# Optimization experiments

Hardware: AMD Instinct MI355X
Metric: run time of the kernel (lower is better)

The kernel has to match this reference:

```python
import jax, jax.numpy as jnp
import numpy as np

NUM_EMBEDDINGS = 1024
EMBEDDING_DIM = 256
COMMITMENT_COST = 0.25


def setup_inputs() -> dict:
    key = jax.random.key(0)
    k1, k2 = jax.random.split(key)
    inputs = jax.random.normal(k1, (64, 1024, EMBEDDING_DIM), dtype=jnp.float32)
    # codebook initialized uniform(-1/K, 1/K) as in the torch module
    embedding = jax.random.uniform(
        k2, (NUM_EMBEDDINGS, EMBEDDING_DIM), dtype=jnp.float32,
        minval=-1.0 / NUM_EMBEDDINGS, maxval=1.0 / NUM_EMBEDDINGS)
    return {"inputs": inputs, "embedding": embedding}


def reference(inputs, embedding):
    # flatten to [N, D]
    D = embedding.shape[1]
    flat = inputs.reshape(-1, D)
    distances = (jnp.sum(flat * flat, axis=1, keepdims=True)
                 + jnp.sum(embedding * embedding, axis=1)
                 - 2.0 * jnp.matmul(flat, embedding.T))
    encoding_indices = jnp.argmin(distances, axis=1)  # [N]
    # one_hot @ embedding == gather; use gather (same math, no NxK one-hot)
    quantized = jnp.take(embedding, encoding_indices, axis=0).reshape(inputs.shape)
    # commitment loss: mse(stop_grad(quantized), inputs)
    e_latent_loss = jnp.mean(jnp.square(jax.lax.stop_gradient(quantized) - inputs))
    loss = COMMITMENT_COST * e_latent_loss
    # straight-through estimator
    quantized = inputs + jax.lax.stop_gradient(quantized - inputs)
    return quantized, loss, encoding_indices.reshape(inputs.shape[:-1])
```

## Files before the change

kernel.cpp:

```cpp
#include <hip/hip_runtime.h>
#include <cfloat>
#include <climits>

#define N_ROWS 65536
#define DIM 256
#define K_CODES 1024
#define N_ELEM 16777216
#define OUT_LOSS_OFF 16777216
#define OUT_IDX_OFF  16777217

#define ROWS_PB 128
#define CT 128
#define EPS_MARGIN 1.5e-4f
#define SHORTLIST_EPS 6e-4f
#define RB 8

#define WS_PARTIALS 0
#define WS_ESQ      8192
#define WS_IDX      12288
#define WS_FLAGCNT  274432
#define WS_FLAGLIST 274436
#define WS_EHI      540672
#define WS_ELO      1064960
#define WS_EHIT     1589248

typedef unsigned short u16;
typedef __attribute__((ext_vector_type(8))) short bf16x8;
typedef __attribute__((ext_vector_type(4))) float f32x4;
typedef union { bf16x8 v; unsigned u[4]; } frag_u;

__device__ __forceinline__ void glds16(const void* g, void* l) {
    __builtin_amdgcn_global_load_lds(
        (const __attribute__((address_space(1))) unsigned int*)g,
        (__attribute__((address_space(3))) unsigned int*)l,
        16, 0, 0);
}

__device__ __forceinline__ unsigned cvt_pk_bf16(float lo, float hi) {
    unsigned r;
    asm("v_cvt_pk_bf16_f32 %0, %1, %2" : "=v"(r) : "v"(lo), "v"(hi));
    return r;
}

__device__ __forceinline__ void split8(float4 a, float4 b, bf16x8& h8, bf16x8& l8) {
    frag_u H, L;
    float f0 = a.x, f1 = a.y, f2 = a.z, f3 = a.w;
    float f4 = b.x, f5 = b.y, f6 = b.z, f7 = b.w;
    const float* f[8] = {&f0,&f1,&f2,&f3,&f4,&f5,&f6,&f7};
    #pragma unroll
    for (int p = 0; p < 4; ++p) {
        float xl = *f[2*p], xh = *f[2*p+1];
        unsigned hw = cvt_pk_bf16(xl, xh);
        float hfl = __uint_as_float(hw << 16);
        float hfh = __uint_as_float(hw & 0xffff0000u);
        H.u[p] = hw;
        L.u[p] = cvt_pk_bf16(xl - hfl, xh - hfh);
    }
    h8 = H.v; l8 = L.v;
}

__device__ __forceinline__ void bsplit(float x, u16& h, u16& l) {
    unsigned u = __float_as_uint(x);
    unsigned hb = (u + 0x7fffu + ((u >> 16) & 1u)) >> 16;
    h = (u16)hb;
    float hf = __uint_as_float(hb << 16);
    float lf = x - hf;
    unsigned u2 = __float_as_uint(lf);
    l = (u16)((u2 + 0x7fffu + ((u2 >> 16) & 1u)) >> 16);
}

__device__ __forceinline__ float np_pairwise_sumsq(const float* __restrict__ a) {
    float half[2];
    #pragma unroll
    for (int h = 0; h < 2; ++h) {
        const float* p = a + h * 128;
        float r[8];
        #pragma unroll
        for (int j = 0; j < 8; ++j) r[j] = __fmul_rn(p[j], p[j]);
        for (int i = 8; i < 128; i += 8) {
            #pragma unroll
            for (int j = 0; j < 8; ++j)
                r[j] = __fadd_rn(r[j], __fmul_rn(p[i + j], p[i + j]));
        }
        half[h] = __fadd_rn(__fadd_rn(__fadd_rn(r[0], r[1]), __fadd_rn(r[2], r[3])),
                            __fadd_rn(__fadd_rn(r[4], r[5]), __fadd_rn(r[6], r[7])));
    }
    return __fadd_rn(half[0], half[1]);
}

__launch_bounds__(256)
__global__ void eprep_kernel(const float* __restrict__ e, u16* __restrict__ ehi,
                             u16* __restrict__ elo, u16* __restrict__ ehiT,
                             float* __restrict__ esqOut, int* __restrict__ flagCnt) {
    const int b = blockIdx.x;
    if (b < 256) {
        int i4 = b * 256 + threadIdx.x;
        float4 v = ((const float4*)e)[i4];
        ushort4 h, l;
        bsplit(v.x, h.x, l.x); bsplit(v.y, h.y, l.y);
        bsplit(v.z, h.z, l.z); bsplit(v.w, h.w, l.w);
        ((ushort4*)ehi)[i4] = h;
        ((ushort4*)elo)[i4] = l;
        int c = i4 >> 6;
        int f4 = i4 & 63;
        int qid = f4 >> 1;
        ((ushort4*)ehiT)[((size_t)qid * 1024 + c) * 2 + (f4 & 1)] = h;
    } else {
        if (b == 256 && threadIdx.x == 0) *flagCnt = 0;
        int c = (b - 256) * 256 + threadIdx.x;
        if (c < K_CODES) esqOut[c] = np_pairwise_sumsq(e + c * DIM);
    }
}

__launch_bounds__(512, 4)
__global__ void argmin_kernel(const float* __restrict__ x,
                              const u16* __restrict__ ehi, const u16* __restrict__ elo,
                              const float* __restrict__ esq, int* __restrict__ wsIdx,
                              int* __restrict__ flagCnt, int* __restrict__ flagList) {
    __shared__ __align__(16) unsigned char lds[65536];
    __shared__ float esq_s[CT];
    u16* xhiS = (u16*)lds;
    u16* xloS = (u16*)(lds + 16384);
    u16* ehiS = (u16*)(lds + 32768);
    u16* eloS = (u16*)(lds + 49152);

    const int t = threadIdx.x;
    const int w = t >> 6;
    const int l = t & 63;
    const int lane15 = l & 15;
    const int quad = l >> 4;
    const int rowBase = blockIdx.x * ROWS_PB;
    const int wr = w >> 1;
    const int wc = w & 1;

    float bv[8], sv[8]; int bi[8];
    #pragma unroll
    for (int i = 0; i < 8; ++i) { bv[i] = FLT_MAX; sv[i] = FLT_MAX; bi[i] = INT_MAX; }

    const int sub8 = l >> 3;
    const int jb8 = l & 7;
    const int sb8 = jb8 ^ sub8;
    const u16* srcE = (w < 6) ? ehi : elo;
    u16* dstE = (w < 6) ? ehiS : eloS;
    const int halfE = w & 1;

    const int g0 = t;
    const int g1 = 512 + t;
    const int r0 = g0 >> 3, jb0 = g0 & 7, sb0 = jb0 ^ (r0 & 7);
    const int r1 = g1 >> 3, jb1 = g1 & 7, sb1 = jb1 ^ (r1 & 7);

    for (int ct = 0; ct < 8; ++ct) {
        const int ctBase = ct * CT;
        __syncthreads();
        if (t < CT) esq_s[t] = esq[ctBase + t];

        f32x4 acc[2][4];
        #pragma unroll
        for (int ti = 0; ti < 2; ++ti)
            #pragma unroll
            for (int tj = 0; tj < 4; ++tj) acc[ti][tj] = (f32x4){0.f, 0.f, 0.f, 0.f};

        for (int ch = 0; ch < 4; ++ch) {
            __syncthreads();
            const float4* gp0 = (const float4*)(x + (size_t)(rowBase + r0) * 256 + ch * 64 + sb0 * 8);
            const float4* gp1 = (const float4*)(x + (size_t)(rowBase + r1) * 256 + ch * 64 + sb1 * 8);
            float4 va0 = gp0[0], vb0 = gp0[1];
            float4 va1 = gp1[0], vb1 = gp1[1];
            if (w >= 4) {
                #pragma unroll
                for (int i = 0; i < 8; ++i) {
                    int r = halfE * 64 + i * 8 + sub8;
                    glds16(srcE + (size_t)(ctBase + r) * 256 + ch * 64 + sb8 * 8,
                           dstE + halfE * 4096 + i * 512);
                }
            }
            {
                bf16x8 h8, l8;
                split8(va0, vb0, h8, l8);
                *(bf16x8*)(xhiS + r0 * 64 + jb0 * 8) = h8;
                *(bf16x8*)(xloS + r0 * 64 + jb0 * 8) = l8;
                split8(va1, vb1, h8, l8);
                *(bf16x8*)(xhiS + r1 * 64 + jb1 * 8) = h8;
                *(bf16x8*)(xloS + r1 * 64 + jb1 * 8) = l8;
            }
            __syncthreads();

            #pragma unroll
            for (int kk = 0; kk < 2; ++kk) {
                bf16x8 ah[2], al4[2], bh[4], bl[4];
                const int blk = kk * 4 + quad;
                #pragma unroll
                for (int ti = 0; ti < 2; ++ti) {
                    int r = wr * 32 + ti * 16 + lane15;
                    int off = r * 64 + ((blk ^ (r & 7)) * 8);
                    ah[ti]  = *(const bf16x8*)(xhiS + off);
                    al4[ti] = *(const bf16x8*)(xloS + off);
                }
                #pragma unroll
                for (int tj = 0; tj < 4; ++tj) {
                    int r = wc * 64 + tj * 16 + lane15;
                    int off = r * 64 + ((blk ^ (r & 7)) * 8);
                    bh[tj] = *(const bf16x8*)(ehiS + off);
                    bl[tj] = *(const bf16x8*)(eloS + off);
                }
                #pragma unroll
                for (int ti = 0; ti < 2; ++ti)
                    #pragma unroll
                    for (int tj = 0; tj < 4; ++tj) {
                        acc[ti][tj] = __builtin_amdgcn_mfma_f32_16x16x32_bf16(al4[ti], bh[tj], acc[ti][tj], 0, 0, 0);
                        acc[ti][tj] = __builtin_amdgcn_mfma_f32_16x16x32_bf16(ah[ti], bl[tj], acc[ti][tj], 0, 0, 0);
                        acc[ti][tj] = __builtin_amdgcn_mfma_f32_16x16x32_bf16(ah[ti], bh[tj], acc[ti][tj], 0, 0, 0);
                    }
            }
        }

        #pragma unroll
        for (int tj = 0; tj < 4; ++tj) {
            int cLoc = wc * 64 + tj * 16 + lane15;
            float cs = esq_s[cLoc];
            int c = ctBase + cLoc;
            #pragma unroll
            for (int ti = 0; ti < 2; ++ti)
                #pragma unroll
                for (int r4 = 0; r4 < 4; ++r4) {
                    int slot = ti * 4 + r4;
                    float s = fmaf(-2.0f, acc[ti][tj][r4], cs);
                    if (s < bv[slot]) {
                        sv[slot] = bv[slot]; bv[slot] = s; bi[slot] = c;
                    } else if (s < sv[slot]) {
                        sv[slot] = s;
                    }
                }
        }
    }

    __syncthreads();
    float* bvA = (float*)lds;
    float* svA = (float*)(lds + 16896);
    int*   biA = (int*)(lds + 33792);
    const int contrib = wc * 16 + lane15;
    #pragma unroll
    for (int slot = 0; slot < 8; ++slot) {
        int m = wr * 32 + (slot >> 2) * 16 + quad * 4 + (slot & 3);
        bvA[m * 33 + contrib] = bv[slot];
        svA[m * 33 + contrib] = sv[slot];
        biA[m * 33 + contrib] = bi[slot];
    }
    __syncthreads();

    if (t < ROWS_PB) {
        float bb = FLT_MAX, ss = FLT_MAX;
        int ii = INT_MAX;
        for (int k = 0; k < 32; ++k) {
            float v  = bvA[t * 33 + k];
            int   id = biA[t * 33 + k];
            float s2 = svA[t * 33 + k];
            if (v < bb || (v == bb && id < ii)) {
                ss = fminf(bb, s2);
                bb = v; ii = id;
            } else {
                ss = fminf(ss, v);
            }
        }
        int row = rowBase + t;
        wsIdx[row] = ii;
        if (ss - bb < EPS_MARGIN) {
            int p = atomicAdd(flagCnt, 1);
            flagList[p] = row;
        }
    }
}

__launch_bounds__(256)
__global__ void rescore_kernel(const float* __restrict__ x, const float* __restrict__ e,
                               const u16* __restrict__ ehiT, const float* __restrict__ esq,
                               int* __restrict__ wsIdx, const int* __restrict__ flagCnt,
                               const int* __restrict__ flagList) {
    __shared__ __align__(16) float xsh[RB][DIM];
    __shared__ float Ash[RB];
    __shared__ float minsh[RB][256];
    __shared__ float thrsh[RB];
    __shared__ int scnt[RB];
    __shared__ int slist[RB][32];
    __shared__ float sres[RB][32];
    const int t = threadIdx.x;
    const int cnt = *flagCnt;
    const int ngroups = (cnt + RB - 1) / RB;
    for (int g = blockIdx.x; g < ngroups; g += gridDim.x) {
        const int base = g * RB;
        const int nr = (cnt - base < RB) ? (cnt - base) : RB;
        __syncthreads();
        #pragma unroll
        for (int r = 0; r < RB; ++r)
            xsh[r][t] = (r < nr) ? x[(size_t)flagList[base + r] * DIM + t] : 0.0f;
        if (t < RB) scnt[t] = 0;
        __syncthreads();
        if (t < RB) Ash[t] = np_pairwise_sumsq(xsh[t]);

        float sA[4][RB];
        #pragma unroll
        for (int j = 0; j < 4; ++j)
            #pragma unroll
            for (int r = 0; r < RB; ++r) sA[j][r] = 0.0f;

        const uint4* eT4 = (const uint4*)ehiT;
        for (int q = 0; q < 32; ++q) {
            float4 xq[RB][2];
            #pragma unroll
            for (int r = 0; r < RB; ++r) {
                xq[r][0] = ((const float4*)xsh[r])[2 * q];
                xq[r][1] = ((const float4*)xsh[r])[2 * q + 1];
            }
            #pragma unroll
            for (int j = 0; j < 4; ++j) {
                uint4 uv = eT4[(size_t)q * 1024 + j * 256 + t];
                float e0 = __uint_as_float(uv.x << 16);
                float e1 = __uint_as_float(uv.x & 0xffff0000u);
                float e2 = __uint_as_float(uv.y << 16);
                float e3 = __uint_as_float(uv.y & 0xffff0000u);
                float e4v = __uint_as_float(uv.z << 16);
                float e5 = __uint_as_float(uv.z & 0xffff0000u);
                float e6 = __uint_as_float(uv.w << 16);
                float e7 = __uint_as_float(uv.w & 0xffff0000u);
                #pragma unroll
                for (int r = 0; r < RB; ++r) {
                    float d0 = sA[j][r];
                    d0 = fmaf(e0, xq[r][0].x, d0);
                    d0 = fmaf(e1, xq[r][0].y, d0);
                    d0 = fmaf(e2, xq[r][0].z, d0);
                    d0 = fmaf(e3, xq[r][0].w, d0);
                    d0 = fmaf(e4v, xq[r][1].x, d0);
                    d0 = fmaf(e5, xq[r][1].y, d0);
                    d0 = fmaf(e6, xq[r][1].z, d0);
                    d0 = fmaf(e7, xq[r][1].w, d0);
                    sA[j][r] = d0;
                }
            }
        }
        #pragma unroll
        for (int j = 0; j < 4; ++j) {
            float cs = esq[j * 256 + t];
            #pragma unroll
            for (int r = 0; r < RB; ++r)
                sA[j][r] = fmaf(-2.0f, sA[j][r], cs);
        }
        #pragma unroll
        for (int r = 0; r < RB; ++r)
            minsh[r][t] = fminf(fminf(sA[0][r], sA[1][r]), fminf(sA[2][r], sA[3][r]));
        __syncthreads();
        for (int off = 128; off > 0; off >>= 1) {
            if (t < off) {
                #pragma unroll
                for (int r = 0; r < RB; ++r)
                    minsh[r][t] = fminf(minsh[r][t], minsh[r][t + off]);
            }
            __syncthreads();
        }
        if (t < RB) thrsh[t] = minsh[t][0] + SHORTLIST_EPS;
        __syncthreads();
        #pragma unroll
        for (int j = 0; j < 4; ++j)
            #pragma unroll
            for (int r = 0; r < RB; ++r)
                if (r < nr && sA[j][r] <= thrsh[r]) {
                    int p = atomicAdd(&scnt[r], 1);
                    if (p < 32) slist[r][p] = j * 256 + t;
                }
        __syncthreads();
        {
            int r = t >> 5, k = t & 31;
            int ns = scnt[r] < 32 ? scnt[r] : 32;
            if (r < nr && k < ns) {
                int c = slist[r][k];
                const float4* ec4 = (const float4*)(e + (size_t)c * DIM);
                const float4* xc4 = (const float4*)xsh[r];
                double dot = 0.0;
                #pragma unroll 8
                for (int d4 = 0; d4 < 64; ++d4) {
                    float4 ev = ec4[d4];
                    float4 xv = xc4[d4];
                    dot += (double)ev.x * (double)xv.x + (double)ev.y * (double)xv.y
                         + (double)ev.z * (double)xv.z + (double)ev.w * (double)xv.w;
                }
                float M = (float)dot;
                sres[r][k] = __fsub_rn(__fadd_rn(Ash[r], esq[c]), __fmul_rn(2.0f, M));
            }
        }
        __syncthreads();
        if (t < nr) {
            int ns = scnt[t] < 32 ? scnt[t] : 32;
            float bb = FLT_MAX; int ii = INT_MAX;
            for (int k = 0; k < ns; ++k) {
                float s = sres[t][k]; int c = slist[t][k];
                if (s < bb || (s == bb && c < ii)) { bb = s; ii = c; }
            }
            wsIdx[flagList[base + t]] = ii;
        }
    }
}

__global__ void gather_kernel(const float* __restrict__ x, const float* __restrict__ e,
                              const int* __restrict__ wsIdx, float* __restrict__ out,
                              double* __restrict__ partials) {
    const float4* x4 = (const float4*)x;
    const float4* e4 = (const float4*)e;
    float4* q4 = (float4*)out;
    float* outIdx = out + OUT_IDX_OFF;
    const int tid = blockIdx.x * 256 + threadIdx.x;
    double sse = 0.0;
    #pragma unroll 4
    for (int i = 0; i < 16; ++i) {
        int u = tid + i * 262144;
        int row = u >> 6;
        int c4 = u & 63;
        int idx = wsIdx[row];
        float4 q = e4[idx * 64 + c4];
        float4 xv = x4[u];
        q4[u] = q;
        double dx = (double)q.x - (double)xv.x;
        double dy = (double)q.y - (double)xv.y;
        double dz = (double)q.z - (double)xv.z;
        double dw = (double)q.w - (double)xv.w;
        sse += dx * dx + dy * dy + dz * dz + dw * dw;
    }
    if (tid < N_ROWS) outIdx[tid] = (float)wsIdx[tid];
    #pragma unroll
    for (int m = 1; m < 64; m <<= 1) sse += __shfl_xor(sse, m);
    __shared__ double wsum[4];
    if ((threadIdx.x & 63) == 0) wsum[threadIdx.x >> 6] = sse;
    __syncthreads();
    if (threadIdx.x == 0)
        partials[blockIdx.x] = wsum[0] + wsum[1] + wsum[2] + wsum[3];
}

__global__ void loss_kernel(const double* __restrict__ partials, float* __restrict__ out) {
    __shared__ double sh[256];
    const int t = threadIdx.x;
    double s = partials[t] + partials[t + 256] + partials[t + 512] + partials[t + 768];
    sh[t] = s;
    __syncthreads();
    for (int off = 128; off > 0; off >>= 1) {
        if (t < off) sh[t] += sh[t + off];
        __syncthreads();
    }
    if (t == 0) out[OUT_LOSS_OFF] = (float)(0.25 * sh[0] / (double)N_ELEM);
}

extern "C" void kernel_launch(void* const* d_in, const int* in_sizes, int n_in,
                              void* d_out, int out_size, void* d_ws, size_t ws_size,
                              hipStream_t stream) {
    (void)in_sizes; (void)n_in; (void)out_size; (void)ws_size;
    const float* x = (const float*)d_in[0];
    const float* e = (const float*)d_in[1];
    float* out = (float*)d_out;
    char* ws = (char*)d_ws;
    double* partials = (double*)(ws + WS_PARTIALS);
    float* esq = (float*)(ws + WS_ESQ);
    int* wsIdx = (int*)(ws + WS_IDX);
    int* flagCnt = (int*)(ws + WS_FLAGCNT);
    int* flagList = (int*)(ws + WS_FLAGLIST);
    u16* ehi = (u16*)(ws + WS_EHI);
    u16* elo = (u16*)(ws + WS_ELO);
    u16* ehiT = (u16*)(ws + WS_EHIT);

    eprep_kernel<<<260, 256, 0, stream>>>(e, ehi, elo, ehiT, esq, flagCnt);
    argmin_kernel<<<N_ROWS / ROWS_PB, 512, 0, stream>>>(x, ehi, elo, esq,
                                                        wsIdx, flagCnt, flagList);
    rescore_kernel<<<512, 256, 0, stream>>>(x, e, ehiT, esq, wsIdx, flagCnt, flagList);
    gather_kernel<<<1024, 256, 0, stream>>>(x, e, wsIdx, out, partials);
    loss_kernel<<<1, 256, 0, stream>>>(partials, out);
}
```

Baseline: 299.8 us.

## Prefetch next x chunk in registers and fold loss reduction into gather

The argmin kernel now loads the next 64-column chunk of x into registers right after the LDS barrier, so the global load overlaps the MFMA work on the current chunk, and the split to bf16 hi/lo is written to LDS at the top of the next iteration. Separately, the standalone loss kernel is removed. The last gather block, detected through an atomic done counter, performs the final reduction, which saves one launch. This costs extra registers for the prefetched values and a threadfence plus an atomic per block.

After: 337.3 us. 1.12x slower.

```diff
diff --git a/kernel.cpp b/kernel.cpp
--- a/kernel.cpp
+++ b/kernel.cpp
@@ -19,7 +19,8 @@
 #define WS_ESQ      8192
 #define WS_IDX      12288
 #define WS_FLAGCNT  274432
-#define WS_FLAGLIST 274436
+#define WS_DONECNT  274436
+#define WS_FLAGLIST 274440
 #define WS_EHI      540672
 #define WS_ELO      1064960
 #define WS_EHIT     1589248
@@ -91,7 +92,8 @@
 __launch_bounds__(256)
 __global__ void eprep_kernel(const float* __restrict__ e, u16* __restrict__ ehi,
                              u16* __restrict__ elo, u16* __restrict__ ehiT,
-                             float* __restrict__ esqOut, int* __restrict__ flagCnt) {
+                             float* __restrict__ esqOut, int* __restrict__ flagCnt,
+                             int* __restrict__ doneCnt) {
     const int b = blockIdx.x;
     if (b < 256) {
         int i4 = b * 256 + threadIdx.x;
@@ -106,7 +108,7 @@
         int qid = f4 >> 1;
         ((ushort4*)ehiT)[((size_t)qid * 1024 + c) * 2 + (f4 & 1)] = h;
     } else {
-        if (b == 256 && threadIdx.x == 0) *flagCnt = 0;
+        if (b == 256 && threadIdx.x == 0) { *flagCnt = 0; *doneCnt = 0; }
         int c = (b - 256) * 256 + threadIdx.x;
         if (c < K_CODES) esqOut[c] = np_pairwise_sumsq(e + c * DIM);
     }
@@ -148,6 +150,12 @@
     const int g1 = 512 + t;
     const int r0 = g0 >> 3, jb0 = g0 & 7, sb0 = jb0 ^ (r0 & 7);
     const int r1 = g1 >> 3, jb1 = g1 & 7, sb1 = jb1 ^ (r1 & 7);
+    const float* xp0 = x + (size_t)(rowBase + r0) * 256 + sb0 * 8;
+    const float* xp1 = x + (size_t)(rowBase + r1) * 256 + sb1 * 8;
+
+    float4 pva0, pvb0, pva1, pvb1;
+    pva0 = ((const float4*)xp0)[0]; pvb0 = ((const float4*)xp0)[1];
+    pva1 = ((const float4*)xp1)[0]; pvb1 = ((const float4*)xp1)[1];
 
     for (int ct = 0; ct < 8; ++ct) {
         const int ctBase = ct * CT;
@@ -162,10 +170,15 @@
 
         for (int ch = 0; ch < 4; ++ch) {
             __syncthreads();
-            const float4* gp0 = (const float4*)(x + (size_t)(rowBase + r0) * 256 + ch * 64 + sb0 * 8);
-            const float4* gp1 = (const float4*)(x + (size_t)(rowBase + r1) * 256 + ch * 64 + sb1 * 8);
-            float4 va0 = gp0[0], vb0 = gp0[1];
-            float4 va1 = gp1[0], vb1 = gp1[1];
+            {
+                bf16x8 h8, l8;
+                split8(pva0, pvb0, h8, l8);
+                *(bf16x8*)(xhiS + r0 * 64 + jb0 * 8) = h8;
+                *(bf16x8*)(xloS + r0 * 64 + jb0 * 8) = l8;
+                split8(pva1, pvb1, h8, l8);
+                *(bf16x8*)(xhiS + r1 * 64 + jb1 * 8) = h8;
+                *(bf16x8*)(xloS + r1 * 64 + jb1 * 8) = l8;
+            }
             if (w >= 4) {
                 #pragma unroll
                 for (int i = 0; i < 8; ++i) {
@@ -174,16 +187,15 @@
                            dstE + halfE * 4096 + i * 512);
                 }
             }
+            __syncthreads();
+
             {
-                bf16x8 h8, l8;
-                split8(va0, vb0, h8, l8);
-                *(bf16x8*)(xhiS + r0 * 64 + jb0 * 8) = h8;
-                *(bf16x8*)(xloS + r0 * 64 + jb0 * 8) = l8;
-                split8(va1, vb1, h8, l8);
-                *(bf16x8*)(xhiS + r1 * 64 + jb1 * 8) = h8;
-                *(bf16x8*)(xloS + r1 * 64 + jb1 * 8) = l8;
-            }
-            __syncthreads();
+                const int chn = (ch + 1) & 3;
+                pva0 = ((const float4*)(xp0 + chn * 64))[0];
+                pvb0 = ((const float4*)(xp0 + chn * 64))[1];
+                pva1 = ((const float4*)(xp1 + chn * 64))[0];
+                pvb1 = ((const float4*)(xp1 + chn * 64))[1];
+            }
 
             #pragma unroll
             for (int kk = 0; kk < 2; ++kk) {
@@ -401,7 +413,7 @@
 
 __global__ void gather_kernel(const float* __restrict__ x, const float* __restrict__ e,
                               const int* __restrict__ wsIdx, float* __restrict__ out,
-                              double* __restrict__ partials) {
+                              double* __restrict__ partials, int* __restrict__ doneCnt) {
     const float4* x4 = (const float4*)x;
     const float4* e4 = (const float4*)e;
     float4* q4 = (float4*)out;
@@ -427,23 +439,31 @@
     #pragma unroll
     for (int m = 1; m < 64; m <<= 1) sse += __shfl_xor(sse, m);
     __shared__ double wsum[4];
+    __shared__ int lastB;
     if ((threadIdx.x & 63) == 0) wsum[threadIdx.x >> 6] = sse;
     __syncthreads();
-    if (threadIdx.x == 0)
+    if (threadIdx.x == 0) {
         partials[blockIdx.x] = wsum[0] + wsum[1] + wsum[2] + wsum[3];
-}
-
-__global__ void loss_kernel(const double* __restrict__ partials, float* __restrict__ out) {
-    __shared__ double sh[256];
-    const int t = threadIdx.x;
-    double s = partials[t] + partials[t + 256] + partials[t + 512] + partials[t + 768];
-    sh[t] = s;
+        __threadfence();
+        unsigned prev = atomicAdd((unsigned*)doneCnt, 1u);
+        lastB = (prev == (unsigned)(gridDim.x - 1)) ? 1 : 0;
+    }
     __syncthreads();
-    for (int off = 128; off > 0; off >>= 1) {
-        if (t < off) sh[t] += sh[t + off];
-        __syncthreads();
-    }
-    if (t == 0) out[OUT_LOSS_OFF] = (float)(0.25 * sh[0] / (double)N_ELEM);
+    if (lastB) {
+        __shared__ double sh[256];
+        const int t = threadIdx.x;
+        double s = __hip_atomic_load(&partials[t],       __ATOMIC_RELAXED, __HIP_MEMORY_SCOPE_AGENT)
+                 + __hip_atomic_load(&partials[t + 256], __ATOMIC_RELAXED, __HIP_MEMORY_SCOPE_AGENT)
+                 + __hip_atomic_load(&partials[t + 512], __ATOMIC_RELAXED, __HIP_MEMORY_SCOPE_AGENT)
+                 + __hip_atomic_load(&partials[t + 768], __ATOMIC_RELAXED, __HIP_MEMORY_SCOPE_AGENT);
+        sh[t] = s;
+        __syncthreads();
+        for (int off = 128; off > 0; off >>= 1) {
+            if (t < off) sh[t] += sh[t + off];
+            __syncthreads();
+        }
+        if (t == 0) out[OUT_LOSS_OFF] = (float)(0.25 * sh[0] / (double)N_ELEM);
+    }
 }
 
 extern "C" void kernel_launch(void* const* d_in, const int* in_sizes, int n_in,
@@ -458,15 +478,15 @@
     float* esq = (float*)(ws + WS_ESQ);
     int* wsIdx = (int*)(ws + WS_IDX);
     int* flagCnt = (int*)(ws + WS_FLAGCNT);
+    int* doneCnt = (int*)(ws + WS_DONECNT);
     int* flagList = (int*)(ws + WS_FLAGLIST);
     u16* ehi = (u16*)(ws + WS_EHI);
     u16* elo = (u16*)(ws + WS_ELO);
     u16* ehiT = (u16*)(ws + WS_EHIT);
 
-    eprep_kernel<<<260, 256, 0, stream>>>(e, ehi, elo, ehiT, esq, flagCnt);
+    eprep_kernel<<<260, 256, 0, stream>>>(e, ehi, elo, ehiT, esq, flagCnt, doneCnt);
     argmin_kernel<<<N_ROWS / ROWS_PB, 512, 0, stream>>>(x, ehi, elo, esq,
                                                         wsIdx, flagCnt, flagList);
     rescore_kernel<<<512, 256, 0, stream>>>(x, e, ehiT, esq, wsIdx, flagCnt, flagList);
-    gather_kernel<<<1024, 256, 0, stream>>>(x, e, wsIdx, out, partials);
-    loss_kernel<<<1, 256, 0, stream>>>(partials, out);
-}
+    gather_kernel<<<1024, 256, 0, stream>>>(x, e, wsIdx, out, partials, doneCnt);
+}
```

## Double-buffer argmin LDS stages with prefetch and single barrier per step

Applied to the files above, without the earlier changes.

Restructures the argmin kernel main loop into a flat 64-step software pipeline over 32-wide K chunks with two LDS buffers. The next x chunk is split and stored, and the next codebook chunk is loaded asynchronously, while MFMAs run on the current buffer. Each step uses one barrier instead of two, and the full esq table is staged once in shared memory. This is meant to hide global-load latency and cut synchronization, at the cost of manual waitcnt handling that is fragile if the counts are wrong.

Result: slower. 325.7 us (+8.6%).

```diff
diff --git a/kernel.cpp b/kernel.cpp
--- a/kernel.cpp
+++ b/kernel.cpp
@@ -118,11 +118,7 @@
                               const float* __restrict__ esq, int* __restrict__ wsIdx,
                               int* __restrict__ flagCnt, int* __restrict__ flagList) {
     __shared__ __align__(16) unsigned char lds[65536];
-    __shared__ float esq_s[CT];
-    u16* xhiS = (u16*)lds;
-    u16* xloS = (u16*)(lds + 16384);
-    u16* ehiS = (u16*)(lds + 32768);
-    u16* eloS = (u16*)(lds + 49152);
+    __shared__ float esqAll[K_CODES];
 
     const int t = threadIdx.x;
     const int w = t >> 6;
@@ -137,104 +133,130 @@
     #pragma unroll
     for (int i = 0; i < 8; ++i) { bv[i] = FLT_MAX; sv[i] = FLT_MAX; bi[i] = INT_MAX; }
 
-    const int sub8 = l >> 3;
-    const int jb8 = l & 7;
-    const int sb8 = jb8 ^ sub8;
-    const u16* srcE = (w < 6) ? ehi : elo;
-    u16* dstE = (w < 6) ? ehiS : eloS;
-    const int halfE = w & 1;
-
-    const int g0 = t;
-    const int g1 = 512 + t;
-    const int r0 = g0 >> 3, jb0 = g0 & 7, sb0 = jb0 ^ (r0 & 7);
-    const int r1 = g1 >> 3, jb1 = g1 & 7, sb1 = jb1 ^ (r1 & 7);
-
-    for (int ct = 0; ct < 8; ++ct) {
-        const int ctBase = ct * CT;
-        __syncthreads();
-        if (t < CT) esq_s[t] = esq[ctBase + t];
-
-        f32x4 acc[2][4];
-        #pragma unroll
-        for (int ti = 0; ti < 2; ++ti)
-            #pragma unroll
-            for (int tj = 0; tj < 4; ++tj) acc[ti][tj] = (f32x4){0.f, 0.f, 0.f, 0.f};
-
-        for (int ch = 0; ch < 4; ++ch) {
-            __syncthreads();
-            const float4* gp0 = (const float4*)(x + (size_t)(rowBase + r0) * 256 + ch * 64 + sb0 * 8);
-            const float4* gp1 = (const float4*)(x + (size_t)(rowBase + r1) * 256 + ch * 64 + sb1 * 8);
-            float4 va0 = gp0[0], vb0 = gp0[1];
-            float4 va1 = gp1[0], vb1 = gp1[1];
-            if (w >= 4) {
+    const int xr = t >> 2, xp = t & 3;
+    const int xg = xp ^ ((xr >> 1) & 3);
+    const float* xptr = x + (size_t)(rowBase + xr) * 256 + xg * 8;
+    const int xoff = xr * 32 + xp * 8;
+
+    const int ec = w * 16 + (l >> 2);
+    const int ep = l & 3;
+    const int eg = ep ^ ((ec >> 1) & 3);
+
+    u16* ldsU = (u16*)lds;
+
+    esqAll[t] = esq[t];
+    esqAll[t + 512] = esq[t + 512];
+    float4 pva, pvb;
+    {
+        const float4* p0 = (const float4*)(xptr + 0);
+        pva = p0[0]; pvb = p0[1];
+        bf16x8 h8, l8;
+        split8(pva, pvb, h8, l8);
+        *(bf16x8*)(ldsU + xoff) = h8;
+        *(bf16x8*)(ldsU + 4096 + xoff) = l8;
+    }
+    glds16(ehi + (size_t)ec * 256 + eg * 8, ldsU + 8192 + w * 512);
+    glds16(elo + (size_t)ec * 256 + eg * 8, ldsU + 12288 + w * 512);
+    asm volatile("" ::: "memory");
+    __builtin_amdgcn_sched_barrier(0);
+    {
+        const float4* p1 = (const float4*)(xptr + 32);
+        pva = p1[0]; pvb = p1[1];
+    }
+    asm volatile("s_waitcnt lgkmcnt(0)" ::: "memory");
+    asm volatile("s_waitcnt vmcnt(2)" ::: "memory");
+    __builtin_amdgcn_sched_barrier(0);
+    __builtin_amdgcn_s_barrier();
+
+    f32x4 acc[2][4];
+    #pragma unroll 2
+    for (int s = 0; s < 64; ++s) {
+        const int sn = (s + 1) & 63;
+        u16* bufC = ldsU + (s & 1) * 16384;
+        u16* bufN = ldsU + (sn & 1) * 16384;
+
+        {
+            bf16x8 h8, l8;
+            split8(pva, pvb, h8, l8);
+            *(bf16x8*)(bufN + xoff) = h8;
+            *(bf16x8*)(bufN + 4096 + xoff) = l8;
+        }
+        {
+            const int ctn = (sn >> 3) * CT;
+            const int chn = (sn & 7) * 32;
+            glds16(ehi + (size_t)(ctn + ec) * 256 + chn + eg * 8, bufN + 8192 + w * 512);
+            glds16(elo + (size_t)(ctn + ec) * 256 + chn + eg * 8, bufN + 12288 + w * 512);
+        }
+        asm volatile("" ::: "memory");
+        __builtin_amdgcn_sched_barrier(0);
+        {
+            const int s2 = (s + 2) & 63;
+            const float4* p = (const float4*)(xptr + (s2 & 7) * 32);
+            pva = p[0]; pvb = p[1];
+        }
+
+        if ((s & 7) == 0) {
+            #pragma unroll
+            for (int ti = 0; ti < 2; ++ti)
                 #pragma unroll
-                for (int i = 0; i < 8; ++i) {
-                    int r = halfE * 64 + i * 8 + sub8;
-                    glds16(srcE + (size_t)(ctBase + r) * 256 + ch * 64 + sb8 * 8,
-                           dstE + halfE * 4096 + i * 512);
-                }
-            }
-            {
-                bf16x8 h8, l8;
-                split8(va0, vb0, h8, l8);
-                *(bf16x8*)(xhiS + r0 * 64 + jb0 * 8) = h8;
-                *(bf16x8*)(xloS + r0 * 64 + jb0 * 8) = l8;
-                split8(va1, vb1, h8, l8);
-                *(bf16x8*)(xhiS + r1 * 64 + jb1 * 8) = h8;
-                *(bf16x8*)(xloS + r1 * 64 + jb1 * 8) = l8;
-            }
-            __syncthreads();
-
-            #pragma unroll
-            for (int kk = 0; kk < 2; ++kk) {
-                bf16x8 ah[2], al4[2], bh[4], bl[4];
-                const int blk = kk * 4 + quad;
-                #pragma unroll
-                for (int ti = 0; ti < 2; ++ti) {
-                    int r = wr * 32 + ti * 16 + lane15;
-                    int off = r * 64 + ((blk ^ (r & 7)) * 8);
-                    ah[ti]  = *(const bf16x8*)(xhiS + off);
-                    al4[ti] = *(const bf16x8*)(xloS + off);
-                }
+                for (int tj = 0; tj < 4; ++tj) acc[ti][tj] = (f32x4){0.f, 0.f, 0.f, 0.f};
+        }
+        {
+            bf16x8 ah[2], al4[2], bh[4], bl[4];
+            #pragma unroll
+            for (int ti = 0; ti < 2; ++ti) {
+                int r = wr * 32 + ti * 16 + lane15;
+                int off = r * 32 + ((quad ^ ((r >> 1) & 3)) * 8);
+                ah[ti]  = *(const bf16x8*)(bufC + off);
+                al4[ti] = *(const bf16x8*)(bufC + 4096 + off);
+            }
+            #pragma unroll
+            for (int tj = 0; tj < 4; ++tj) {
+                int c = wc * 64 + tj * 16 + lane15;
+                int off = c * 32 + ((quad ^ ((c >> 1) & 3)) * 8);
+                bh[tj] = *(const bf16x8*)(bufC + 8192 + off);
+                bl[tj] = *(const bf16x8*)(bufC + 12288 + off);
+            }
+            #pragma unroll
+            for (int ti = 0; ti < 2; ++ti)
                 #pragma unroll
                 for (int tj = 0; tj < 4; ++tj) {
-                    int r = wc * 64 + tj * 16 + lane15;
-                    int off = r * 64 + ((blk ^ (r & 7)) * 8);
-                    bh[tj] = *(const bf16x8*)(ehiS + off);
-                    bl[tj] = *(const bf16x8*)(eloS + off);
+                    acc[ti][tj] = __builtin_amdgcn_mfma_f32_16x16x32_bf16(al4[ti], bh[tj], acc[ti][tj], 0, 0, 0);
+                    acc[ti][tj] = __builtin_amdgcn_mfma_f32_16x16x32_bf16(ah[ti], bl[tj], acc[ti][tj], 0, 0, 0);
+                    acc[ti][tj] = __builtin_amdgcn_mfma_f32_16x16x32_bf16(ah[ti], bh[tj], acc[ti][tj], 0, 0, 0);
                 }
+        }
+        if ((s & 7) == 7) {
+            const int ctBase = (s >> 3) * CT;
+            #pragma unroll
+            for (int tj = 0; tj < 4; ++tj) {
+                int cLoc = wc * 64 + tj * 16 + lane15;
+                int c = ctBase + cLoc;
+                float cs = esqAll[c];
                 #pragma unroll
                 for (int ti = 0; ti < 2; ++ti)
                     #pragma unroll
-                    for (int tj = 0; tj < 4; ++tj) {
-                        acc[ti][tj] = __builtin_amdgcn_mfma_f32_16x16x32_bf16(al4[ti], bh[tj], acc[ti][tj], 0, 0, 0);
-                        acc[ti][tj] = __builtin_amdgcn_mfma_f32_16x16x32_bf16(ah[ti], bl[tj], acc[ti][tj], 0, 0, 0);
-                        acc[ti][tj] = __builtin_amdgcn_mfma_f32_16x16x32_bf16(ah[ti], bh[tj], acc[ti][tj], 0, 0, 0);
+                    for (int r4 = 0; r4 < 4; ++r4) {
+                        int slot = ti * 4 + r4;
+                        float sc = fmaf(-2.0f, acc[ti][tj][r4], cs);
+                        if (sc < bv[slot]) {
+                            sv[slot] = bv[slot]; bv[slot] = sc; bi[slot] = c;
+                        } else if (sc < sv[slot]) {
+                            sv[slot] = sc;
+                        }
                     }
             }
         }
 
-        #pragma unroll
-        for (int tj = 0; tj < 4; ++tj) {
-            int cLoc = wc * 64 + tj * 16 + lane15;
-            float cs = esq_s[cLoc];
-            int c = ctBase + cLoc;
-            #pragma unroll
-            for (int ti = 0; ti < 2; ++ti)
-                #pragma unroll
-                for (int r4 = 0; r4 < 4; ++r4) {
-                    int slot = ti * 4 + r4;
-                    float s = fmaf(-2.0f, acc[ti][tj][r4], cs);
-                    if (s < bv[slot]) {
-                        sv[slot] = bv[slot]; bv[slot] = s; bi[slot] = c;
-                    } else if (s < sv[slot]) {
-                        sv[slot] = s;
-                    }
-                }
-        }
-    }
-
-    __syncthreads();
+        asm volatile("s_waitcnt lgkmcnt(0)" ::: "memory");
+        asm volatile("s_waitcnt vmcnt(2)" ::: "memory");
+        __builtin_amdgcn_sched_barrier(0);
+        __builtin_amdgcn_s_barrier();
+    }
+
+    asm volatile("s_waitcnt vmcnt(0) lgkmcnt(0)" ::: "memory");
+    __builtin_amdgcn_s_barrier();
+
     float* bvA = (float*)lds;
     float* svA = (float*)(lds + 16896);
     int*   biA = (int*)(lds + 33792);
```

## Collect near-best candidates in argmin pass to skip full rescore scan

Applied to the files above, without the earlier changes.

While computing the approximate distances, the argmin kernel now keeps a per-row candidate list in LDS. The threshold is the running row minimum plus a small margin, tracked with ordered-uint atomicMin. For flagged ambiguous rows the lists are written to scratch space inside the output buffer. The rescore kernel then runs exact double-precision dot products only on those candidates, with a full 1024-code fallback when a list overflows, replacing the bf16 full-codebook scan and the transposed codebook copy. This adds LDS atomics and an extra __syncthreads per code tile inside the hot argmin loop. The threshold uses the running minimum, so candidates found before a later, better minimum can fill the list.

Result: faster. 289.2 us (-3.6%).

```diff
diff --git a/kernel.cpp b/kernel.cpp
--- a/kernel.cpp
+++ b/kernel.cpp
@@ -12,7 +12,8 @@
 #define ROWS_PB 128
 #define CT 128
 #define EPS_MARGIN 1.5e-4f
-#define SHORTLIST_EPS 6e-4f
+#define CAND_TH 1.0e-4f
+#define CAND_CAP 24
 #define RB 8
 
 #define WS_PARTIALS 0
@@ -22,7 +23,6 @@
 #define WS_FLAGLIST 274436
 #define WS_EHI      540672
 #define WS_ELO      1064960
-#define WS_EHIT     1589248
 
 typedef unsigned short u16;
 typedef __attribute__((ext_vector_type(8))) short bf16x8;
@@ -69,6 +69,14 @@
     l = (u16)((u2 + 0x7fffu + ((u2 >> 16) & 1u)) >> 16);
 }
 
+__device__ __forceinline__ unsigned ford(float f) {
+    unsigned u = __float_as_uint(f);
+    return (u & 0x80000000u) ? ~u : (u | 0x80000000u);
+}
+__device__ __forceinline__ float finv(unsigned o) {
+    return __uint_as_float((o & 0x80000000u) ? (o ^ 0x80000000u) : ~o);
+}
+
 __device__ __forceinline__ float np_pairwise_sumsq(const float* __restrict__ a) {
     float half[2];
     #pragma unroll
@@ -90,8 +98,8 @@
 
 __launch_bounds__(256)
 __global__ void eprep_kernel(const float* __restrict__ e, u16* __restrict__ ehi,
-                             u16* __restrict__ elo, u16* __restrict__ ehiT,
-                             float* __restrict__ esqOut, int* __restrict__ flagCnt) {
+                             u16* __restrict__ elo, float* __restrict__ esqOut,
+                             int* __restrict__ flagCnt) {
     const int b = blockIdx.x;
     if (b < 256) {
         int i4 = b * 256 + threadIdx.x;
@@ -101,10 +109,6 @@
         bsplit(v.z, h.z, l.z); bsplit(v.w, h.w, l.w);
         ((ushort4*)ehi)[i4] = h;
         ((ushort4*)elo)[i4] = l;
-        int c = i4 >> 6;
-        int f4 = i4 & 63;
-        int qid = f4 >> 1;
-        ((ushort4*)ehiT)[((size_t)qid * 1024 + c) * 2 + (f4 & 1)] = h;
     } else {
         if (b == 256 && threadIdx.x == 0) *flagCnt = 0;
         int c = (b - 256) * 256 + threadIdx.x;
@@ -116,9 +120,13 @@
 __global__ void argmin_kernel(const float* __restrict__ x,
                               const u16* __restrict__ ehi, const u16* __restrict__ elo,
                               const float* __restrict__ esq, int* __restrict__ wsIdx,
-                              int* __restrict__ flagCnt, int* __restrict__ flagList) {
+                              int* __restrict__ flagCnt, int* __restrict__ flagList,
+                              int* __restrict__ wsCand, int* __restrict__ wsCnt) {
     __shared__ __align__(16) unsigned char lds[65536];
     __shared__ float esq_s[CT];
+    __shared__ unsigned rowBestOrd[ROWS_PB];
+    __shared__ int candCnt[ROWS_PB];
+    __shared__ int candList[ROWS_PB][CAND_CAP];
     u16* xhiS = (u16*)lds;
     u16* xloS = (u16*)(lds + 16384);
     u16* ehiS = (u16*)(lds + 32768);
@@ -137,6 +145,8 @@
     #pragma unroll
     for (int i = 0; i < 8; ++i) { bv[i] = FLT_MAX; sv[i] = FLT_MAX; bi[i] = INT_MAX; }
 
+    if (t < ROWS_PB) { rowBestOrd[t] = 0xFFFFFFFFu; candCnt[t] = 0; }
+
     const int sub8 = l >> 3;
     const int jb8 = l & 7;
     const int sb8 = jb8 ^ sub8;
@@ -214,6 +224,9 @@
             }
         }
 
+        float sl[8];
+        #pragma unroll
+        for (int i = 0; i < 8; ++i) sl[i] = FLT_MAX;
         #pragma unroll
         for (int tj = 0; tj < 4; ++tj) {
             int cLoc = wc * 64 + tj * 16 + lane15;
@@ -230,8 +243,33 @@
                     } else if (s < sv[slot]) {
                         sv[slot] = s;
                     }
-                }
-        }
+                    sl[slot] = fminf(sl[slot], s);
+                }
+        }
+        #pragma unroll
+        for (int ti = 0; ti < 2; ++ti)
+            #pragma unroll
+            for (int r4 = 0; r4 < 4; ++r4) {
+                int m = wr * 32 + ti * 16 + quad * 4 + r4;
+                atomicMin(&rowBestOrd[m], ford(sl[ti * 4 + r4]));
+            }
+        __syncthreads();
+        #pragma unroll
+        for (int ti = 0; ti < 2; ++ti)
+            #pragma unroll
+            for (int r4 = 0; r4 < 4; ++r4) {
+                int m = wr * 32 + ti * 16 + quad * 4 + r4;
+                float th = finv(rowBestOrd[m]) + CAND_TH;
+                #pragma unroll
+                for (int tj = 0; tj < 4; ++tj) {
+                    int cLoc = wc * 64 + tj * 16 + lane15;
+                    float s = fmaf(-2.0f, acc[ti][tj][r4], esq_s[cLoc]);
+                    if (s < th) {
+                        int p = atomicAdd(&candCnt[m], 1);
+                        if (p < CAND_CAP) candList[m][p] = ctBase + cLoc;
+                    }
+                }
+            }
     }
 
     __syncthreads();
@@ -267,22 +305,26 @@
         if (ss - bb < EPS_MARGIN) {
             int p = atomicAdd(flagCnt, 1);
             flagList[p] = row;
+            int cc = candCnt[t];
+            wsCnt[row] = cc;
+            int n = cc < CAND_CAP ? cc : CAND_CAP;
+            for (int k = 0; k < n; ++k) wsCand[row * CAND_CAP + k] = candList[t][k];
         }
     }
 }
 
 __launch_bounds__(256)
 __global__ void rescore_kernel(const float* __restrict__ x, const float* __restrict__ e,
-                               const u16* __restrict__ ehiT, const float* __restrict__ esq,
-                               int* __restrict__ wsIdx, const int* __restrict__ flagCnt,
-                               const int* __restrict__ flagList) {
+                               const float* __restrict__ esq, int* __restrict__ wsIdx,
+                               const int* __restrict__ flagCnt, const int* __restrict__ flagList,
+                               const int* __restrict__ wsCand, const int* __restrict__ wsCnt) {
     __shared__ __align__(16) float xsh[RB][DIM];
     __shared__ float Ash[RB];
-    __shared__ float minsh[RB][256];
-    __shared__ float thrsh[RB];
-    __shared__ int scnt[RB];
-    __shared__ int slist[RB][32];
-    __shared__ float sres[RB][32];
+    __shared__ int rowsh[RB];
+    __shared__ int cntsh[RB];
+    __shared__ float sres[RB][CAND_CAP + 8];
+    __shared__ float ovS[256];
+    __shared__ int ovC[256];
     const int t = threadIdx.x;
     const int cnt = *flagCnt;
     const int ngroups = (cnt + RB - 1) / RB;
@@ -290,88 +332,24 @@
         const int base = g * RB;
         const int nr = (cnt - base < RB) ? (cnt - base) : RB;
         __syncthreads();
+        if (t < RB) {
+            int row = flagList[base + ((t < nr) ? t : 0)];
+            rowsh[t] = row;
+            cntsh[t] = (t < nr) ? wsCnt[row] : 0;
+        }
+        __syncthreads();
         #pragma unroll
         for (int r = 0; r < RB; ++r)
-            xsh[r][t] = (r < nr) ? x[(size_t)flagList[base + r] * DIM + t] : 0.0f;
-        if (t < RB) scnt[t] = 0;
+            xsh[r][t] = x[(size_t)rowsh[r] * DIM + t];
         __syncthreads();
         if (t < RB) Ash[t] = np_pairwise_sumsq(xsh[t]);
-
-        float sA[4][RB];
-        #pragma unroll
-        for (int j = 0; j < 4; ++j)
-            #pragma unroll
-            for (int r = 0; r < RB; ++r) sA[j][r] = 0.0f;
-
-        const uint4* eT4 = (const uint4*)ehiT;
-        for (int q = 0; q < 32; ++q) {
-            float4 xq[RB][2];
-            #pragma unroll
-            for (int r = 0; r < RB; ++r) {
-                xq[r][0] = ((const float4*)xsh[r])[2 * q];
-                xq[r][1] = ((const float4*)xsh[r])[2 * q + 1];
-            }
-            #pragma unroll
-            for (int j = 0; j < 4; ++j) {
-                uint4 uv = eT4[(size_t)q * 1024 + j * 256 + t];
-                float e0 = __uint_as_float(uv.x << 16);
-                float e1 = __uint_as_float(uv.x & 0xffff0000u);
-                float e2 = __uint_as_float(uv.y << 16);
-                float e3 = __uint_as_float(uv.y & 0xffff0000u);
-                float e4v = __uint_as_float(uv.z << 16);
-                float e5 = __uint_as_float(uv.z & 0xffff0000u);
-                float e6 = __uint_as_float(uv.w << 16);
-                float e7 = __uint_as_float(uv.w & 0xffff0000u);
-                #pragma unroll
-                for (int r = 0; r < RB; ++r) {
-                    float d0 = sA[j][r];
-                    d0 = fmaf(e0, xq[r][0].x, d0);
-                    d0 = fmaf(e1, xq[r][0].y, d0);
-                    d0 = fmaf(e2, xq[r][0].z, d0);
-                    d0 = fmaf(e3, xq[r][0].w, d0);
-                    d0 = fmaf(e4v, xq[r][1].x, d0);
-                    d0 = fmaf(e5, xq[r][1].y, d0);
-                    d0 = fmaf(e6, xq[r][1].z, d0);
-                    d0 = fmaf(e7, xq[r][1].w, d0);
-                    sA[j][r] = d0;
-                }
-            }
-        }
-        #pragma unroll
-        for (int j = 0; j < 4; ++j) {
-            float cs = esq[j * 256 + t];
-            #pragma unroll
-            for (int r = 0; r < RB; ++r)
-                sA[j][r] = fmaf(-2.0f, sA[j][r], cs);
-        }
-        #pragma unroll
-        for (int r = 0; r < RB; ++r)
-            minsh[r][t] = fminf(fminf(sA[0][r], sA[1][r]), fminf(sA[2][r], sA[3][r]));
-        __syncthreads();
-        for (int off = 128; off > 0; off >>= 1) {
-            if (t < off) {
-                #pragma unroll
-                for (int r = 0; r < RB; ++r)
-                    minsh[r][t] = fminf(minsh[r][t], minsh[r][t + off]);
-            }
-            __syncthreads();
-        }
-        if (t < RB) thrsh[t] = minsh[t][0] + SHORTLIST_EPS;
-        __syncthreads();
-        #pragma unroll
-        for (int j = 0; j < 4; ++j)
-            #pragma unroll
-            for (int r = 0; r < RB; ++r)
-                if (r < nr && sA[j][r] <= thrsh[r]) {
-                    int p = atomicAdd(&scnt[r], 1);
-                    if (p < 32) slist[r][p] = j * 256 + t;
-                }
-        __syncthreads();
+        __syncthreads();
+
         {
             int r = t >> 5, k = t & 31;
-            int ns = scnt[r] < 32 ? scnt[r] : 32;
-            if (r < nr && k < ns) {
-                int c = slist[r][k];
+            int nc = (cntsh[r] <= CAND_CAP) ? cntsh[r] : 0;
+            if (r < nr && k < nc) {
+                int c = wsCand[(size_t)rowsh[r] * CAND_CAP + k];
                 const float4* ec4 = (const float4*)(e + (size_t)c * DIM);
                 const float4* xc4 = (const float4*)xsh[r];
                 double dot = 0.0;
@@ -387,14 +365,46 @@
             }
         }
         __syncthreads();
-        if (t < nr) {
-            int ns = scnt[t] < 32 ? scnt[t] : 32;
+        if (t < nr && cntsh[t] <= CAND_CAP) {
+            int nc = cntsh[t];
             float bb = FLT_MAX; int ii = INT_MAX;
-            for (int k = 0; k < ns; ++k) {
-                float s = sres[t][k]; int c = slist[t][k];
+            for (int k = 0; k < nc; ++k) {
+                float s = sres[t][k];
+                int c = wsCand[(size_t)rowsh[t] * CAND_CAP + k];
                 if (s < bb || (s == bb && c < ii)) { bb = s; ii = c; }
             }
-            wsIdx[flagList[base + t]] = ii;
+            wsIdx[rowsh[t]] = ii;
+        }
+        for (int r = 0; r < nr; ++r) {
+            if (cntsh[r] <= CAND_CAP) continue;
+            __syncthreads();
+            float bs = FLT_MAX; int bc = INT_MAX;
+            for (int j = 0; j < 4; ++j) {
+                int c = j * 256 + t;
+                const float4* ec4 = (const float4*)(e + (size_t)c * DIM);
+                const float4* xc4 = (const float4*)xsh[r];
+                double dot = 0.0;
+                #pragma unroll 8
+                for (int d4 = 0; d4 < 64; ++d4) {
+                    float4 ev = ec4[d4];
+                    float4 xv = xc4[d4];
+                    dot += (double)ev.x * (double)xv.x + (double)ev.y * (double)xv.y
+                         + (double)ev.z * (double)xv.z + (double)ev.w * (double)xv.w;
+                }
+                float M = (float)dot;
+                float s = __fsub_rn(__fadd_rn(Ash[r], esq[c]), __fmul_rn(2.0f, M));
+                if (s < bs || (s == bs && c < bc)) { bs = s; bc = c; }
+            }
+            ovS[t] = bs; ovC[t] = bc;
+            __syncthreads();
+            for (int off = 128; off > 0; off >>= 1) {
+                if (t < off) {
+                    float s2 = ovS[t + off]; int c2 = ovC[t + off];
+                    if (s2 < ovS[t] || (s2 == ovS[t] && c2 < ovC[t])) { ovS[t] = s2; ovC[t] = c2; }
+                }
+                __syncthreads();
+            }
+            if (t == 0) wsIdx[rowsh[r]] = ovC[0];
         }
     }
 }
@@ -461,12 +471,14 @@
     int* flagList = (int*)(ws + WS_FLAGLIST);
     u16* ehi = (u16*)(ws + WS_EHI);
     u16* elo = (u16*)(ws + WS_ELO);
-    u16* ehiT = (u16*)(ws + WS_EHIT);
-
-    eprep_kernel<<<260, 256, 0, stream>>>(e, ehi, elo, ehiT, esq, flagCnt);
-    argmin_kernel<<<N_ROWS / ROWS_PB, 512, 0, stream>>>(x, ehi, elo, esq,
-                                                        wsIdx, flagCnt, flagList);
-    rescore_kernel<<<512, 256, 0, stream>>>(x, e, ehiT, esq, wsIdx, flagCnt, flagList);
+    int* wsCand = (int*)d_out;
+    int* wsCnt = wsCand + (size_t)N_ROWS * CAND_CAP;
+
+    eprep_kernel<<<260, 256, 0, stream>>>(e, ehi, elo, esq, flagCnt);
+    argmin_kernel<<<N_ROWS / ROWS_PB, 512, 0, stream>>>(x, ehi, elo, esq, wsIdx,
+                                                        flagCnt, flagList, wsCand, wsCnt);
+    rescore_kernel<<<512, 256, 0, stream>>>(x, e, esq, wsIdx, flagCnt, flagList,
+                                            wsCand, wsCnt);
     gather_kernel<<<1024, 256, 0, stream>>>(x, e, wsIdx, out, partials);
     loss_kernel<<<1, 256, 0, stream>>>(partials, out);
 }
```
